# Kernel optimization log

Hardware: AMD Instinct MI355X
Metric: run time of the kernel (lower is better)

Reference implementation:

```python
import jax, jax.numpy as jnp
import numpy as np

B, C, H, W = 16, 512, 64, 64
K = 32


def setup_inputs() -> dict:
    key = jax.random.key(0)
    k1, k2, k3 = jax.random.split(key, 3)
    std = 1.0 / (64 * C) ** 0.5
    x = jax.random.normal(k1, (B, C, H, W), dtype=jnp.float32)
    codewords = jax.random.uniform(k2, (K, C), dtype=jnp.float32, minval=-std, maxval=std)
    scale = jax.random.uniform(k3, (K,), dtype=jnp.float32, minval=-1.0, maxval=0.0)
    return {"x": x, "codewords": codewords, "scale": scale}


def reference(x, codewords, scale):
    b, c, h, w = x.shape
    # (b, n, c) with n = h*w spatial positions
    xf = x.reshape(b, c, h * w).transpose(0, 2, 1)
    x2 = jnp.sum(xf * xf, axis=-1)                       # (b, n)
    c2 = jnp.sum(codewords * codewords, axis=-1)          # (k,)
    xc = jnp.einsum('bnc,kc->bnk', xf, codewords)         # (b, n, k)
    logits = scale[None, None, :] * (x2[:, :, None] - 2.0 * xc + c2[None, None, :])
    A = jax.nn.softmax(logits, axis=2)                    # (b, n, k)
    # sum_n A[b,n,k] * (x[b,n,c] - codewords[k,c])
    encoded = jnp.einsum('bnk,bnc->bkc', A, xf) - jnp.einsum('bnk,kc->bkc', A, codewords)
    return encoded
```

## Files before the change

### kernel.cpp

```cpp
#include <hip/hip_runtime.h>
#include <hip/hip_bf16.h>
#include <math.h>

#define BB 16
#define CC 512
#define NN 4096
#define KK 32

typedef __attribute__((ext_vector_type(8))) short short8;
typedef __attribute__((ext_vector_type(4))) short short4v;
typedef __attribute__((ext_vector_type(4))) float float4v;

static __device__ __forceinline__ unsigned short f2bf(float f) {
  unsigned u = __float_as_uint(f);
  u += 0x7FFF + ((u >> 16) & 1);
  return (unsigned short)(u >> 16);
}

static __device__ __forceinline__ short8 cat8(short4v a, short4v b) {
  short8 r;
  r[0] = a[0]; r[1] = a[1]; r[2] = a[2]; r[3] = a[3];
  r[4] = b[0]; r[5] = b[1]; r[6] = b[2]; r[7] = b[3];
  return r;
}


__global__ __launch_bounds__(256) void prep_kernel(
    const float* __restrict__ cw, unsigned short* __restrict__ cwP,
    float* __restrict__ c2, float* __restrict__ asum) {
  int gid = blockIdx.x * 256 + threadIdx.x;
  if (gid < BB * KK) asum[gid] = 0.f;
  {
    int k = gid >> 9;
    int cc = gid & 511;
    int cs = cc & ~31;
    int w5 = cc & 31;
    int q = w5 >> 3, j = w5 & 7;
    int src_c = cs + 2 * q + (j & 1) + ((j >> 1) << 3);
    cwP[gid] = f2bf(cw[k * CC + src_c]);
  }
  __shared__ float c2p[KK][8];
  if (blockIdx.x == 0) {
    int k = threadIdx.x >> 3, j = threadIdx.x & 7;
    const float* row = cw + k * CC + j * 64;
    float s = 0.f;
    for (int i = 0; i < 64; ++i) s = fmaf(row[i], row[i], s);
    c2p[k][j] = s;
    __syncthreads();
    if (threadIdx.x < KK) {
      float t = 0.f;
      for (int j2 = 0; j2 < 8; ++j2) t += c2p[threadIdx.x][j2];
      c2[threadIdx.x] = t;
    }
  }
}

#define XP2 36
__global__ __launch_bounds__(256, 4) void fused_kernel(
    const float* __restrict__ x, const unsigned short* __restrict__ cwP,
    const float* __restrict__ c2g, const float* __restrict__ scale,
    float* __restrict__ partials, float* __restrict__ asum) {
  const int b = blockIdx.x >> 5;
  const int chunk = blockIdx.x & 31;
  const int t = threadIdx.x;
  const int w = t >> 6;
  const int l = t & 63;
  const int l15 = l & 15;
  const int q = l >> 4;
  const int wrole = (w + ((blockIdx.x & 1) << 1)) & 3;

  __shared__ unsigned short Xl[CC * XP2];
  __shared__ unsigned short As[KK * XP2];
  __shared__ float Sx2w[4 * 32];
  __shared__ float Sx2[32];

  const float* xb0 = x + (size_t)b * CC * NN + chunk * 128;

  const float sc0 = scale[l15], sc1 = scale[16 + l15];
  const float cc0 = c2g[l15], cc1 = c2g[16 + l15];

  float4v acc[8][2];
#pragma unroll
  for (int ct = 0; ct < 8; ++ct)
#pragma unroll
    for (int m = 0; m < 2; ++m) acc[ct][m] = (float4v){0.f, 0.f, 0.f, 0.f};
  float s0acc = 0.f, s1acc = 0.f;

  const int f4 = t & 7;
  const int cr = t >> 3;

  for (int sub = 0; sub < 4; ++sub) {
    const float* xb = xb0 + sub * 32;

    float4v x2p = (float4v){0.f, 0.f, 0.f, 0.f};
#pragma unroll 8
    for (int i = 0; i < 16; ++i) {
      const int c = cr + 32 * i;
      float4v v = *(const float4v*)(xb + (size_t)c * NN + 4 * f4);
      x2p.x = fmaf(v.x, v.x, x2p.x);
      x2p.y = fmaf(v.y, v.y, x2p.y);
      x2p.z = fmaf(v.z, v.z, x2p.z);
      x2p.w = fmaf(v.w, v.w, x2p.w);
      unsigned p0 = (unsigned)f2bf(v.x) | ((unsigned)f2bf(v.y) << 16);
      unsigned p1 = (unsigned)f2bf(v.z) | ((unsigned)f2bf(v.w) << 16);
      *(uint2*)&Xl[c * XP2 + 4 * f4] = make_uint2(p0, p1);
    }
#pragma unroll
    for (int m = 8; m <= 32; m <<= 1) {
      x2p.x += __shfl_xor(x2p.x, m);
      x2p.y += __shfl_xor(x2p.y, m);
      x2p.z += __shfl_xor(x2p.z, m);
      x2p.w += __shfl_xor(x2p.w, m);
    }
    if (l < 8) *(float4v*)&Sx2w[w * 32 + 4 * l] = x2p;
    __syncthreads();

    float4v p0 = (float4v){0.f, 0.f, 0.f, 0.f};
    float4v p1 = (float4v){0.f, 0.f, 0.f, 0.f};
    if (wrole < 2) {
      const int nrow = wrole * 16 + l15;
      for (int cs = 0; cs < 512; cs += 32) {
        const int cb2 = cs + 2 * q;
        short8 af;
#pragma unroll
        for (int j = 0; j < 8; ++j) {
          const int c = cb2 + (j & 1) + ((j >> 1) << 3);
          af[j] = (short)Xl[c * XP2 + nrow];
        }
        short8 b0 = *(const short8*)(cwP + (size_t)l15 * CC + cs + q * 8);
        short8 b1 = *(const short8*)(cwP + (size_t)(16 + l15) * CC + cs + q * 8);
        p0 = __builtin_amdgcn_mfma_f32_16x16x32_bf16(af, b0, p0, 0, 0, 0);
        p1 = __builtin_amdgcn_mfma_f32_16x16x32_bf16(af, b1, p1, 0, 0, 0);
      }
    } else if (wrole == 2 && l < 32) {
      Sx2[l] = Sx2w[l] + Sx2w[32 + l] + Sx2w[64 + l] + Sx2w[96 + l];
    }
    __syncthreads();

    if (wrole < 2) {
      float a0[4], a1[4];
#pragma unroll
      for (int r = 0; r < 4; ++r) {
        const float xx = Sx2[wrole * 16 + 4 * q + r];
        float l0 = sc0 * (xx - 2.f * p0[r] + cc0);
        float l1 = sc1 * (xx - 2.f * p1[r] + cc1);
        float m = fmaxf(l0, l1);
        m = fmaxf(m, __shfl_xor(m, 1));
        m = fmaxf(m, __shfl_xor(m, 2));
        m = fmaxf(m, __shfl_xor(m, 4));
        m = fmaxf(m, __shfl_xor(m, 8));
        float e0 = __expf(l0 - m), e1 = __expf(l1 - m);
        float s = e0 + e1;
        s += __shfl_xor(s, 1);
        s += __shfl_xor(s, 2);
        s += __shfl_xor(s, 4);
        s += __shfl_xor(s, 8);
        float inv = 1.0f / s;
        a0[r] = e0 * inv;
        a1[r] = e1 * inv;
      }
      s0acc += a0[0] + a0[1] + a0[2] + a0[3];
      s1acc += a1[0] + a1[1] + a1[2] + a1[3];
      unsigned p00 = (unsigned)f2bf(a0[0]) | ((unsigned)f2bf(a0[1]) << 16);
      unsigned p01 = (unsigned)f2bf(a0[2]) | ((unsigned)f2bf(a0[3]) << 16);
      unsigned p10 = (unsigned)f2bf(a1[0]) | ((unsigned)f2bf(a1[1]) << 16);
      unsigned p11 = (unsigned)f2bf(a1[2]) | ((unsigned)f2bf(a1[3]) << 16);
      const int nc = wrole * 16 + 4 * q;
      *(uint2*)&As[l15 * XP2 + nc] = make_uint2(p00, p01);
      *(uint2*)&As[(16 + l15) * XP2 + nc] = make_uint2(p10, p11);
    }
    __syncthreads();

    {
      const int nb = q * 8;
      const short4v* Ap0 = (const short4v*)&As[l15 * XP2 + nb];
      const short4v* Ap1 = (const short4v*)&As[(16 + l15) * XP2 + nb];
      short8 am0 = cat8(Ap0[0], Ap0[1]);
      short8 am1 = cat8(Ap1[0], Ap1[1]);
#pragma unroll
      for (int ct = 0; ct < 8; ++ct) {
        const int c = w * 128 + ct * 16 + l15;
        const short4v* Bp = (const short4v*)&Xl[c * XP2 + nb];
        short8 bx = cat8(Bp[0], Bp[1]);
        acc[ct][0] = __builtin_amdgcn_mfma_f32_16x16x32_bf16(am0, bx, acc[ct][0], 0, 0, 0);
        acc[ct][1] = __builtin_amdgcn_mfma_f32_16x16x32_bf16(am1, bx, acc[ct][1], 0, 0, 0);
      }
    }
    __syncthreads();
  }

  float* pout = partials + (size_t)blockIdx.x * KK * CC;
#pragma unroll
  for (int ct = 0; ct < 8; ++ct) {
    const int c = w * 128 + ct * 16 + l15;
#pragma unroll
    for (int m = 0; m < 2; ++m)
#pragma unroll
      for (int r = 0; r < 4; ++r) {
        int k = 16 * m + 4 * q + r;
        pout[k * CC + c] = acc[ct][m][r];
      }
  }
  s0acc += __shfl_xor(s0acc, 16);
  s0acc += __shfl_xor(s0acc, 32);
  s1acc += __shfl_xor(s1acc, 16);
  s1acc += __shfl_xor(s1acc, 32);
  if (wrole < 2 && q == 0) {
    atomicAdd(&asum[b * KK + l15], s0acc);
    atomicAdd(&asum[b * KK + 16 + l15], s1acc);
  }
}

__global__ __launch_bounds__(256) void reduce_kernel(
    const float* __restrict__ partials, const float* __restrict__ asum,
    const float* __restrict__ cw, float* __restrict__ out) {
  int idx = blockIdx.x * 256 + threadIdx.x;
  int b = idx >> 12;
  int k = (idx >> 7) & 31;
  int c4 = idx & 127;

  float4v o = {0.f, 0.f, 0.f, 0.f};
  const float4v* pb = (const float4v*)partials + ((size_t)(b * 32) * KK + k) * 128 + c4;
#pragma unroll 8
  for (int p = 0; p < 32; ++p) {
    float4v v = pb[(size_t)p * KK * 128];
    o.x += v.x;
    o.y += v.y;
    o.z += v.z;
    o.w += v.w;
  }
  float4v wv = ((const float4v*)cw)[k * 128 + c4];
  float a = asum[b * KK + k];
  o.x -= a * wv.x;
  o.y -= a * wv.y;
  o.z -= a * wv.z;
  o.w -= a * wv.w;
  ((float4v*)out)[idx] = o;
}

extern "C" void kernel_launch(void* const* d_in, const int* in_sizes, int n_in,
                              void* d_out, int out_size, void* d_ws, size_t ws_size,
                              hipStream_t stream) {
  const float* x = (const float*)d_in[0];
  const float* cw = (const float*)d_in[1];
  const float* scale = (const float*)d_in[2];
  float* out = (float*)d_out;
  char* ws = (char*)d_ws;

  float* c2 = (float*)ws;
  unsigned short* cwP = (unsigned short*)(ws + 128);
  float* asum = (float*)(ws + 32896);
  float* partials = (float*)(ws + 35072);

  prep_kernel<<<64, 256, 0, stream>>>(cw, cwP, c2, asum);
  fused_kernel<<<512, 256, 0, stream>>>(x, cwP, c2, scale, partials, asum);
  reduce_kernel<<<256, 256, 0, stream>>>(partials, asum, cw, out);
}
```

Measured before the change: 231.6 us.

## Double grid size and replace partial-sum buffer with global atomic accumulation

The fused kernel now launches 1024 blocks, each covering 64 spatial positions instead of 128, which raises parallelism across the GPU. Each block atomically adds its per-(k,c) results into a per-batch accumulator, zeroed in the prep kernel, instead of writing a full partial slab per block. The separate 32-way reduction kernel becomes a light finalize pass. The cost is 64-way atomic contention on every output element plus duplicated per-block setup, and the float summation order is no longer deterministic.

Result: slower. 260.7 us (+12.6%).

```diff
diff --git a/kernel.cpp b/kernel.cpp
--- a/kernel.cpp
+++ b/kernel.cpp
@@ -27,9 +27,16 @@
 
 __global__ __launch_bounds__(256) void prep_kernel(
     const float* __restrict__ cw, unsigned short* __restrict__ cwP,
-    float* __restrict__ c2, float* __restrict__ asum) {
+    float* __restrict__ c2, float* __restrict__ asum,
+    float* __restrict__ accum) {
   int gid = blockIdx.x * 256 + threadIdx.x;
   if (gid < BB * KK) asum[gid] = 0.f;
+  {
+    float4v z = {0.f, 0.f, 0.f, 0.f};
+    float4v* a4 = (float4v*)accum + (size_t)gid * 4;
+#pragma unroll
+    for (int i = 0; i < 4; ++i) a4[i] = z;
+  }
   {
     int k = gid >> 9;
     int cc = gid & 511;
@@ -59,23 +66,22 @@
 __global__ __launch_bounds__(256, 4) void fused_kernel(
     const float* __restrict__ x, const unsigned short* __restrict__ cwP,
     const float* __restrict__ c2g, const float* __restrict__ scale,
-    float* __restrict__ partials, float* __restrict__ asum) {
-  const int b = blockIdx.x >> 5;
-  const int chunk = blockIdx.x & 31;
+    float* __restrict__ accum, float* __restrict__ asum) {
+  const int b = blockIdx.x >> 6;
+  const int chunk = blockIdx.x & 63;
   const int t = threadIdx.x;
   const int w = t >> 6;
   const int l = t & 63;
   const int l15 = l & 15;
   const int q = l >> 4;
-  const int wrole = (w + ((blockIdx.x & 1) << 1)) & 3;
+  const int wrole = (w + (blockIdx.x & 3)) & 3;
 
   __shared__ unsigned short Xl[CC * XP2];
   __shared__ unsigned short As[KK * XP2];
   __shared__ float Sx2w[4 * 32];
   __shared__ float Sx2[32];
 
-  const float* xb0 = x + (size_t)b * CC * NN + chunk * 128;
-
+  const float* xb0 = x + (size_t)b * CC * NN + chunk * 64;
   const float sc0 = scale[l15], sc1 = scale[16 + l15];
   const float cc0 = c2g[l15], cc1 = c2g[16 + l15];
 
@@ -89,7 +95,7 @@
   const int f4 = t & 7;
   const int cr = t >> 3;
 
-  for (int sub = 0; sub < 4; ++sub) {
+  for (int sub = 0; sub < 2; ++sub) {
     const float* xb = xb0 + sub * 32;
 
     float4v x2p = (float4v){0.f, 0.f, 0.f, 0.f};
@@ -189,7 +195,7 @@
     __syncthreads();
   }
 
-  float* pout = partials + (size_t)blockIdx.x * KK * CC;
+  float* aout = accum + (size_t)b * KK * CC;
 #pragma unroll
   for (int ct = 0; ct < 8; ++ct) {
     const int c = w * 128 + ct * 16 + l15;
@@ -198,7 +204,7 @@
 #pragma unroll
       for (int r = 0; r < 4; ++r) {
         int k = 16 * m + 4 * q + r;
-        pout[k * CC + c] = acc[ct][m][r];
+        atomicAdd(&aout[k * CC + c], acc[ct][m][r]);
       }
   }
   s0acc += __shfl_xor(s0acc, 16);
@@ -211,31 +217,22 @@
   }
 }
 
-__global__ __launch_bounds__(256) void reduce_kernel(
-    const float* __restrict__ partials, const float* __restrict__ asum,
+__global__ __launch_bounds__(256) void finalize_kernel(
+    const float* __restrict__ accum, const float* __restrict__ asum,
     const float* __restrict__ cw, float* __restrict__ out) {
-  int idx = blockIdx.x * 256 + threadIdx.x;
-  int b = idx >> 12;
-  int k = (idx >> 7) & 31;
-  int c4 = idx & 127;
-
-  float4v o = {0.f, 0.f, 0.f, 0.f};
-  const float4v* pb = (const float4v*)partials + ((size_t)(b * 32) * KK + k) * 128 + c4;
-#pragma unroll 8
-  for (int p = 0; p < 32; ++p) {
-    float4v v = pb[(size_t)p * KK * 128];
-    o.x += v.x;
-    o.y += v.y;
-    o.z += v.z;
-    o.w += v.w;
-  }
+  int o = blockIdx.x * 256 + threadIdx.x;
+  int b = o >> 12;
+  int k = (o >> 7) & 31;
+  int c4 = o & 127;
+
+  float4v s = ((const float4v*)accum)[o];
   float4v wv = ((const float4v*)cw)[k * 128 + c4];
   float a = asum[b * KK + k];
-  o.x -= a * wv.x;
-  o.y -= a * wv.y;
-  o.z -= a * wv.z;
-  o.w -= a * wv.w;
-  ((float4v*)out)[idx] = o;
+  s.x -= a * wv.x;
+  s.y -= a * wv.y;
+  s.z -= a * wv.z;
+  s.w -= a * wv.w;
+  ((float4v*)out)[o] = s;
 }
 
 extern "C" void kernel_launch(void* const* d_in, const int* in_sizes, int n_in,
@@ -250,9 +247,9 @@
   float* c2 = (float*)ws;
   unsigned short* cwP = (unsigned short*)(ws + 128);
   float* asum = (float*)(ws + 32896);
-  float* partials = (float*)(ws + 35072);
-
-  prep_kernel<<<64, 256, 0, stream>>>(cw, cwP, c2, asum);
-  fused_kernel<<<512, 256, 0, stream>>>(x, cwP, c2, scale, partials, asum);
-  reduce_kernel<<<256, 256, 0, stream>>>(partials, asum, cw, out);
-}
+  float* accum = (float*)(ws + 35072);
+
+  prep_kernel<<<64, 256, 0, stream>>>(cw, cwP, c2, asum, accum);
+  fused_kernel<<<1024, 256, 0, stream>>>(x, cwP, c2, scale, accum, asum);
+  finalize_kernel<<<256, 256, 0, stream>>>(accum, asum, cw, out);
+}
```
